# Optimization experiments

Hardware: AMD Instinct MI355X
Metric: run time of the kernel (lower is better)

The kernel has to match this reference:

```python
import jax, jax.numpy as jnp
import numpy as np

EPS = 1e-8


def setup_inputs() -> dict:
    key = jax.random.key(0)
    k1, k2, k3, k4, k5 = jax.random.split(key, 5)
    B, D, N, M = 16, 128, 2048, 2048
    return {
        "src_embedding": jax.random.normal(k1, (B, D, N), dtype=jnp.float32),
        "tgt_embedding": jax.random.normal(k2, (B, D, M), dtype=jnp.float32),
        "src": jax.random.normal(k3, (B, 3, N), dtype=jnp.float32),
        "tgt": jax.random.normal(k4, (B, 3, M), dtype=jnp.float32),
        "temperature": jax.random.uniform(k5, (B, 1), dtype=jnp.float32),
    }


def reference(src_embedding, tgt_embedding, src, tgt, temperature):
    B = src.shape[0]
    # cross-attention scores [B, N, M] and row softmax
    scores = jax.nn.softmax(
        jnp.einsum("bdn,bdm->bnm", src_embedding, tgt_embedding), axis=-1
    )
    # hard correspondence: argmax over tgt points, gather tgt coords -> [B, 3, N]
    idx = jnp.argmax(scores, axis=-1)                      # [B, N]
    src_corr = jnp.take_along_axis(tgt, idx[:, None, :].repeat(3, axis=1), axis=-1)
    # entropy-based weights (note: original applies -1/(entropy+eps), kept faithfully)
    w = jnp.sum(scores * jnp.log(scores + EPS), axis=-1)   # [B, N]
    w = -1.0 / (w + EPS)
    w_norm = w / (jnp.sum(w, axis=-1, keepdims=True) + EPS)  # [B, N]
    wn = w_norm[:, None, :]                                # [B, 1, N]
    src_centroid = jnp.sum(src * wn, axis=2, keepdims=True)       # [B, 3, 1]
    tgt_centroid = jnp.sum(src_corr * wn, axis=2, keepdims=True)  # [B, 3, 1]
    src_centered = src - src_centroid
    corr_centered = (src_corr - tgt_centroid) * wn
    # 3x3 cross-covariance per batch
    H = jnp.einsum("bin,bjn->bij", src_centered, corr_centered) + jnp.eye(3, dtype=src.dtype) * EPS
    # batched 3x3 SVD entirely on device; torch.svd returns V s.t. H = U S V^T
    U, S, Vh = jnp.linalg.svd(H)
    V = jnp.swapaxes(Vh, -1, -2)
    r = jnp.einsum("bij,bkj->bik", V, U)                   # V @ U^T
    det = jnp.linalg.det(r)                                # [B]
    diag = jnp.tile(jnp.eye(3, dtype=src.dtype), (B, 1, 1)).at[:, 2, 2].set(det)
    R = jnp.einsum("bij,bjk,blk->bil", V, diag, U)         # V @ diag @ U^T
    t = (jnp.einsum("bij,bjk->bik", -R, src_centroid) + tgt_centroid).reshape(B, 3)
    return R, t, scores
```

## Files before the change

### kernel.cpp

```cpp
#include <hip/hip_runtime.h>
#include <math.h>

constexpr int B = 16, D = 128, N = 2048, M = 2048;
#define EPSF 1e-8f

__global__ __launch_bounds__(256) void gemm_logits(
    const float* __restrict__ Ae, const float* __restrict__ Be,
    float* __restrict__ out)
{
    const int b  = blockIdx.z;
    const int n0 = blockIdx.y * 128;
    const int m0 = blockIdx.x * 128;
    const float* A  = Ae + (size_t)b * D * N;
    const float* Bm = Be + (size_t)b * D * M;
    float* C = out + (size_t)b * N * M;

    __shared__ float As[8][128];
    __shared__ float Bs[8][128];

    const int t  = threadIdx.x;
    const int lr = t >> 5;
    const int lc = (t & 31) * 4;
    const int tx = t & 15;
    const int ty = t >> 4;

    float acc[8][8];
#pragma unroll
    for (int i = 0; i < 8; ++i)
#pragma unroll
        for (int j = 0; j < 8; ++j) acc[i][j] = 0.f;

    for (int d0 = 0; d0 < D; d0 += 8) {
        const float4 av = *(const float4*)(A  + (size_t)(d0 + lr) * N + n0 + lc);
        const float4 bv = *(const float4*)(Bm + (size_t)(d0 + lr) * M + m0 + lc);
        *(float4*)(&As[lr][lc]) = av;
        *(float4*)(&Bs[lr][lc]) = bv;
        __syncthreads();
#pragma unroll
        for (int kk = 0; kk < 8; ++kk) {
            float a[8], bb[8];
            *(float4*)(&a[0])  = *(const float4*)(&As[kk][ty * 4]);
            *(float4*)(&a[4])  = *(const float4*)(&As[kk][64 + ty * 4]);
            *(float4*)(&bb[0]) = *(const float4*)(&Bs[kk][tx * 4]);
            *(float4*)(&bb[4]) = *(const float4*)(&Bs[kk][64 + tx * 4]);
#pragma unroll
            for (int i = 0; i < 8; ++i)
#pragma unroll
                for (int j = 0; j < 8; ++j)
                    acc[i][j] = fmaf(a[i], bb[j], acc[i][j]);
        }
        __syncthreads();
    }

#pragma unroll
    for (int i = 0; i < 8; ++i) {
        const int row = (i < 4) ? (ty * 4 + i) : (64 + ty * 4 + (i - 4));
        float4 c0 = make_float4(acc[i][0], acc[i][1], acc[i][2], acc[i][3]);
        float4 c1 = make_float4(acc[i][4], acc[i][5], acc[i][6], acc[i][7]);
        size_t base = (size_t)(n0 + row) * M + m0;
        *(float4*)(C + base + tx * 4)      = c0;
        *(float4*)(C + base + 64 + tx * 4) = c1;
    }
}

__global__ __launch_bounds__(256) void softmax_rows(
    float* __restrict__ scores, float* __restrict__ wout, int* __restrict__ idxout)
{
    const int row = blockIdx.x;
    float* p = scores + (size_t)row * M;
    const int t = threadIdx.x;

    float4 v0 = ((const float4*)p)[t];
    float4 v1 = ((const float4*)p)[t + 256];
    float vals[8] = {v0.x, v0.y, v0.z, v0.w, v1.x, v1.y, v1.z, v1.w};
    int   idxs[8] = {t*4, t*4+1, t*4+2, t*4+3,
                     1024 + t*4, 1024 + t*4 + 1, 1024 + t*4 + 2, 1024 + t*4 + 3};

    float m = vals[0]; int mi = idxs[0];
#pragma unroll
    for (int k = 1; k < 8; ++k)
        if (vals[k] > m) { m = vals[k]; mi = idxs[k]; }

    __shared__ float sv[256];
    __shared__ int   si[256];
    sv[t] = m; si[t] = mi;
    __syncthreads();
    for (int s = 128; s > 0; s >>= 1) {
        if (t < s) {
            float ov = sv[t + s]; int oi = si[t + s];
            if (ov > sv[t] || (ov == sv[t] && oi < si[t])) { sv[t] = ov; si[t] = oi; }
        }
        __syncthreads();
    }
    const float rowmax = sv[0];
    const int   rowidx = si[0];
    __syncthreads();

    float e[8]; float lsum = 0.f;
#pragma unroll
    for (int k = 0; k < 8; ++k) { e[k] = expf(vals[k] - rowmax); lsum += e[k]; }
    sv[t] = lsum;
    __syncthreads();
    for (int s = 128; s > 0; s >>= 1) { if (t < s) sv[t] += sv[t + s]; __syncthreads(); }
    const float inv = 1.0f / sv[0];
    __syncthreads();

    float ent = 0.f;
#pragma unroll
    for (int k = 0; k < 8; ++k) {
        float pk = e[k] * inv;
        e[k] = pk;
        ent += pk * logf(pk + EPSF);
    }
    ((float4*)p)[t]       = make_float4(e[0], e[1], e[2], e[3]);
    ((float4*)p)[t + 256] = make_float4(e[4], e[5], e[6], e[7]);

    sv[t] = ent;
    __syncthreads();
    for (int s = 128; s > 0; s >>= 1) { if (t < s) sv[t] += sv[t + s]; __syncthreads(); }
    if (t == 0) {
        wout[row]   = -1.0f / (sv[0] + EPSF);
        idxout[row] = rowidx;
    }
}

__device__ inline float block_sum_256(float v, float* red, int t)
{
    red[t] = v; __syncthreads();
    for (int s = 128; s > 0; s >>= 1) { if (t < s) red[t] += red[t + s]; __syncthreads(); }
    float r = red[0]; __syncthreads();
    return r;
}

__global__ __launch_bounds__(256) void kabsch(
    const float* __restrict__ src, const float* __restrict__ tgt,
    const float* __restrict__ wraw, const int* __restrict__ idxv,
    float* __restrict__ Rout, float* __restrict__ tout)
{
    const int b = blockIdx.x;
    const int t = threadIdx.x;
    const float* S  = src  + (size_t)b * 3 * N;
    const float* T  = tgt  + (size_t)b * 3 * M;
    const float* w  = wraw + (size_t)b * N;
    const int*  idx = idxv + (size_t)b * N;

    __shared__ float red[256];

    float w8[8]; int i8[8];
    float s8[8][3], g8[8][3];
    float lsum = 0.f;
#pragma unroll
    for (int k = 0; k < 8; ++k) {
        int n = t + 256 * k;
        w8[k] = w[n];
        i8[k] = idx[n];
        lsum += w8[k];
#pragma unroll
        for (int i = 0; i < 3; ++i) {
            s8[k][i] = S[i * N + n];
            g8[k][i] = T[i * M + i8[k]];
        }
    }
    const float W = block_sum_256(lsum, red, t) + EPSF;

    float c[6] = {0, 0, 0, 0, 0, 0};
#pragma unroll
    for (int k = 0; k < 8; ++k) {
        float wn = w8[k] / W;
#pragma unroll
        for (int i = 0; i < 3; ++i) {
            c[i]     += wn * s8[k][i];
            c[3 + i] += wn * g8[k][i];
        }
    }
    float cen[6];
    for (int i = 0; i < 6; ++i) cen[i] = block_sum_256(c[i], red, t);

    float h[9] = {0};
#pragma unroll
    for (int k = 0; k < 8; ++k) {
        float wn = w8[k] / W;
        float a0 = s8[k][0] - cen[0], a1 = s8[k][1] - cen[1], a2 = s8[k][2] - cen[2];
        float b0 = (g8[k][0] - cen[3]) * wn;
        float b1 = (g8[k][1] - cen[4]) * wn;
        float b2 = (g8[k][2] - cen[5]) * wn;
        h[0] += a0 * b0; h[1] += a0 * b1; h[2] += a0 * b2;
        h[3] += a1 * b0; h[4] += a1 * b1; h[5] += a1 * b2;
        h[6] += a2 * b0; h[7] += a2 * b1; h[8] += a2 * b2;
    }
    float hr[9];
    for (int i = 0; i < 9; ++i) hr[i] = block_sum_256(h[i], red, t);

    if (t == 0) {
        double H[3][3];
        for (int i = 0; i < 3; ++i)
            for (int j = 0; j < 3; ++j)
                H[i][j] = (double)hr[i * 3 + j] + (i == j ? 1e-8 : 0.0);

        double A[3][3];
        for (int i = 0; i < 3; ++i)
            for (int j = 0; j < 3; ++j)
                A[i][j] = H[0][i] * H[0][j] + H[1][i] * H[1][j] + H[2][i] * H[2][j];

        double V[3][3] = {{1, 0, 0}, {0, 1, 0}, {0, 0, 1}};
        const int PP[3] = {0, 0, 1}, QQ[3] = {1, 2, 2};
        for (int sweep = 0; sweep < 30; ++sweep) {
            for (int r = 0; r < 3; ++r) {
                int p = PP[r], q = QQ[r];
                double apq = A[p][q];
                if (fabs(apq) < 1e-300) continue;
                double theta = (A[q][q] - A[p][p]) / (2.0 * apq);
                double tt = (theta >= 0 ? 1.0 : -1.0) /
                            (fabs(theta) + sqrt(theta * theta + 1.0));
                double cc = 1.0 / sqrt(tt * tt + 1.0);
                double ss = tt * cc;
                for (int k = 0; k < 3; ++k) {
                    double akp = A[k][p], akq = A[k][q];
                    A[k][p] = cc * akp - ss * akq;
                    A[k][q] = ss * akp + cc * akq;
                }
                for (int k = 0; k < 3; ++k) {
                    double apk = A[p][k], aqk = A[q][k];
                    A[p][k] = cc * apk - ss * aqk;
                    A[q][k] = ss * apk + cc * aqk;
                }
                for (int k = 0; k < 3; ++k) {
                    double vkp = V[k][p], vkq = V[k][q];
                    V[k][p] = cc * vkp - ss * vkq;
                    V[k][q] = ss * vkp + cc * vkq;
                }
            }
        }
        double ev[3] = {A[0][0], A[1][1], A[2][2]};
        int ord[3] = {0, 1, 2};
        for (int i = 0; i < 2; ++i)
            for (int j = i + 1; j < 3; ++j)
                if (ev[ord[j]] > ev[ord[i]]) { int tmp = ord[i]; ord[i] = ord[j]; ord[j] = tmp; }
        double Vs[3][3];
        for (int i = 0; i < 3; ++i)
            for (int j = 0; j < 3; ++j)
                Vs[i][j] = V[i][ord[j]];

        double U[3][3];
        for (int j = 0; j < 2; ++j) {
            double u0 = H[0][0] * Vs[0][j] + H[0][1] * Vs[1][j] + H[0][2] * Vs[2][j];
            double u1 = H[1][0] * Vs[0][j] + H[1][1] * Vs[1][j] + H[1][2] * Vs[2][j];
            double u2 = H[2][0] * Vs[0][j] + H[2][1] * Vs[1][j] + H[2][2] * Vs[2][j];
            if (j == 1) {
                double d0 = u0 * U[0][0] + u1 * U[1][0] + u2 * U[2][0];
                u0 -= d0 * U[0][0]; u1 -= d0 * U[1][0]; u2 -= d0 * U[2][0];
            }
            double nn = sqrt(u0 * u0 + u1 * u1 + u2 * u2);
            if (nn < 1e-150) {
                u0 = (j == 0) ? 1.0 : -U[1][0];
                u1 = (j == 0) ? 0.0 : U[0][0];
                u2 = 0.0;
                nn = sqrt(u0 * u0 + u1 * u1 + u2 * u2);
                if (nn < 1e-150) { u0 = 0; u1 = 0; u2 = 1; nn = 1; }
            }
            U[0][j] = u0 / nn; U[1][j] = u1 / nn; U[2][j] = u2 / nn;
        }
        U[0][2] = U[1][0] * U[2][1] - U[2][0] * U[1][1];
        U[1][2] = U[2][0] * U[0][1] - U[0][0] * U[2][1];
        U[2][2] = U[0][0] * U[1][1] - U[1][0] * U[0][1];

        double r[3][3];
        for (int i = 0; i < 3; ++i)
            for (int j = 0; j < 3; ++j)
                r[i][j] = Vs[i][0] * U[j][0] + Vs[i][1] * U[j][1] + Vs[i][2] * U[j][2];
        double det = r[0][0] * (r[1][1] * r[2][2] - r[1][2] * r[2][1])
                   - r[0][1] * (r[1][0] * r[2][2] - r[1][2] * r[2][0])
                   + r[0][2] * (r[1][0] * r[2][1] - r[1][1] * r[2][0]);

        double R[3][3];
        for (int i = 0; i < 3; ++i)
            for (int j = 0; j < 3; ++j)
                R[i][j] = Vs[i][0] * U[j][0] + Vs[i][1] * U[j][1] + det * Vs[i][2] * U[j][2];

        double tv[3];
        for (int i = 0; i < 3; ++i)
            tv[i] = (double)cen[3 + i]
                  - (R[i][0] * cen[0] + R[i][1] * cen[1] + R[i][2] * cen[2]);

        for (int i = 0; i < 3; ++i)
            for (int j = 0; j < 3; ++j)
                Rout[b * 9 + i * 3 + j] = (float)R[i][j];
        for (int i = 0; i < 3; ++i)
            tout[b * 3 + i] = (float)tv[i];
    }
}

extern "C" void kernel_launch(void* const* d_in, const int* in_sizes, int n_in,
                              void* d_out, int out_size, void* d_ws, size_t ws_size,
                              hipStream_t stream)
{
    const float* src_emb = (const float*)d_in[0];
    const float* tgt_emb = (const float*)d_in[1];
    const float* src     = (const float*)d_in[2];
    const float* tgt     = (const float*)d_in[3];

    float* out    = (float*)d_out;
    float* Rout   = out;
    float* tout   = out + B * 9;
    float* scores = out + B * 12;

    float* wws   = (float*)d_ws;
    int*   idxws = (int*)((float*)d_ws + B * N);

    dim3 g1(M / 128, N / 128, B);
    gemm_logits<<<g1, 256, 0, stream>>>(src_emb, tgt_emb, scores);
    softmax_rows<<<B * N, 256, 0, stream>>>(scores, wws, idxws);
    kabsch<<<B, 256, 0, stream>>>(src, tgt, wws, idxws, Rout, tout);
}
```

Baseline: 572.1 us.

## Prefetch next GEMM tile into registers and use wave-shuffle block reductions

```diff
diff --git a/kernel.cpp b/kernel.cpp
--- a/kernel.cpp
+++ b/kernel.cpp
@@ -24,18 +24,26 @@
     const int tx = t & 15;
     const int ty = t >> 4;
 
+    const float* Aptr = A  + (size_t)lr * N + n0 + lc;
+    const float* Bptr = Bm + (size_t)lr * M + m0 + lc;
+
     float acc[8][8];
 #pragma unroll
     for (int i = 0; i < 8; ++i)
 #pragma unroll
         for (int j = 0; j < 8; ++j) acc[i][j] = 0.f;
 
+    float4 av = *(const float4*)(Aptr);
+    float4 bv = *(const float4*)(Bptr);
+
     for (int d0 = 0; d0 < D; d0 += 8) {
-        const float4 av = *(const float4*)(A  + (size_t)(d0 + lr) * N + n0 + lc);
-        const float4 bv = *(const float4*)(Bm + (size_t)(d0 + lr) * M + m0 + lc);
         *(float4*)(&As[lr][lc]) = av;
         *(float4*)(&Bs[lr][lc]) = bv;
         __syncthreads();
+        if (d0 + 8 < D) {
+            av = *(const float4*)(Aptr + (size_t)(d0 + 8) * N);
+            bv = *(const float4*)(Bptr + (size_t)(d0 + 8) * M);
+        }
 #pragma unroll
         for (int kk = 0; kk < 8; ++kk) {
             float a[8], bb[8];
@@ -69,6 +77,7 @@
     const int row = blockIdx.x;
     float* p = scores + (size_t)row * M;
     const int t = threadIdx.x;
+    const int wid = t >> 6;
 
     float4 v0 = ((const float4*)p)[t];
     float4 v1 = ((const float4*)p)[t + 256];
@@ -83,27 +92,49 @@
 
     __shared__ float sv[256];
     __shared__ int   si[256];
+    __shared__ float resf[2];
+    __shared__ int   resi;
+
     sv[t] = m; si[t] = mi;
     __syncthreads();
-    for (int s = 128; s > 0; s >>= 1) {
-        if (t < s) {
-            float ov = sv[t + s]; int oi = si[t + s];
-            if (ov > sv[t] || (ov == sv[t] && oi < si[t])) { sv[t] = ov; si[t] = oi; }
-        }
-        __syncthreads();
-    }
-    const float rowmax = sv[0];
-    const int   rowidx = si[0];
-    __syncthreads();
+    if (t < 128) {
+        float ov = sv[t + 128]; int oi = si[t + 128];
+        if (ov > m || (ov == m && oi < mi)) { m = ov; mi = oi; }
+    }
+    if (wid == 1) { sv[t] = m; si[t] = mi; }
+    __syncthreads();
+    if (t < 64) {
+        float ov = sv[t + 64]; int oi = si[t + 64];
+        if (ov > m || (ov == m && oi < mi)) { m = ov; mi = oi; }
+#pragma unroll
+        for (int s = 32; s > 0; s >>= 1) {
+            float om = __shfl_down(m, s);
+            int   oi2 = __shfl_down(mi, s);
+            if (om > m || (om == m && oi2 < mi)) { m = om; mi = oi2; }
+        }
+        if (t == 0) { resf[0] = m; resi = mi; }
+    }
+    __syncthreads();
+    const float rowmax = resf[0];
+    const int   rowidx = resi;
 
     float e[8]; float lsum = 0.f;
 #pragma unroll
     for (int k = 0; k < 8; ++k) { e[k] = expf(vals[k] - rowmax); lsum += e[k]; }
     sv[t] = lsum;
     __syncthreads();
-    for (int s = 128; s > 0; s >>= 1) { if (t < s) sv[t] += sv[t + s]; __syncthreads(); }
-    const float inv = 1.0f / sv[0];
-    __syncthreads();
+    float sum = lsum;
+    if (t < 128) sum = sum + sv[t + 128];
+    if (wid == 1) sv[t] = sum;
+    __syncthreads();
+    if (t < 64) {
+        sum = sum + sv[t + 64];
+#pragma unroll
+        for (int s = 32; s > 0; s >>= 1) sum = sum + __shfl_down(sum, s);
+        if (t == 0) resf[1] = sum;
+    }
+    __syncthreads();
+    const float inv = 1.0f / resf[1];
 
     float ent = 0.f;
 #pragma unroll
@@ -117,19 +148,51 @@
 
     sv[t] = ent;
     __syncthreads();
-    for (int s = 128; s > 0; s >>= 1) { if (t < s) sv[t] += sv[t + s]; __syncthreads(); }
-    if (t == 0) {
-        wout[row]   = -1.0f / (sv[0] + EPSF);
-        idxout[row] = rowidx;
-    }
-}
-
-__device__ inline float block_sum_256(float v, float* red, int t)
-{
-    red[t] = v; __syncthreads();
-    for (int s = 128; s > 0; s >>= 1) { if (t < s) red[t] += red[t + s]; __syncthreads(); }
-    float r = red[0]; __syncthreads();
-    return r;
+    if (t < 128) ent = ent + sv[t + 128];
+    if (wid == 1) sv[t] = ent;
+    __syncthreads();
+    if (t < 64) {
+        ent = ent + sv[t + 64];
+#pragma unroll
+        for (int s = 32; s > 0; s >>= 1) ent = ent + __shfl_down(ent, s);
+        if (t == 0) {
+            wout[row]   = -1.0f / (ent + EPSF);
+            idxout[row] = rowidx;
+        }
+    }
+}
+
+template <int Q>
+__device__ inline void block_sum_hybrid(float (&v)[Q], float (*red)[256],
+                                        float* res, int t, int wid)
+{
+#pragma unroll
+    for (int q = 0; q < Q; ++q) red[q][t] = v[q];
+    __syncthreads();
+    if (t < 128) {
+#pragma unroll
+        for (int q = 0; q < Q; ++q) v[q] += red[q][t + 128];
+    }
+    if (wid == 1) {
+#pragma unroll
+        for (int q = 0; q < Q; ++q) red[q][t] = v[q];
+    }
+    __syncthreads();
+    if (t < 64) {
+#pragma unroll
+        for (int q = 0; q < Q; ++q) v[q] += red[q][t + 64];
+#pragma unroll
+        for (int s = 32; s > 0; s >>= 1)
+#pragma unroll
+            for (int q = 0; q < Q; ++q) v[q] += __shfl_down(v[q], s);
+        if (t == 0) {
+#pragma unroll
+            for (int q = 0; q < Q; ++q) res[q] = v[q];
+        }
+    }
+    __syncthreads();
+#pragma unroll
+    for (int q = 0; q < Q; ++q) v[q] = res[q];
 }
 
 __global__ __launch_bounds__(256) void kabsch(
@@ -139,29 +202,32 @@
 {
     const int b = blockIdx.x;
     const int t = threadIdx.x;
+    const int wid = t >> 6;
     const float* S  = src  + (size_t)b * 3 * N;
     const float* T  = tgt  + (size_t)b * 3 * M;
     const float* w  = wraw + (size_t)b * N;
     const int*  idx = idxv + (size_t)b * N;
 
-    __shared__ float red[256];
+    __shared__ float red[9][256];
+    __shared__ float res[9];
 
     float w8[8]; int i8[8];
     float s8[8][3], g8[8][3];
-    float lsum = 0.f;
+    float lsum[1] = {0.f};
 #pragma unroll
     for (int k = 0; k < 8; ++k) {
         int n = t + 256 * k;
         w8[k] = w[n];
         i8[k] = idx[n];
-        lsum += w8[k];
+        lsum[0] += w8[k];
 #pragma unroll
         for (int i = 0; i < 3; ++i) {
             s8[k][i] = S[i * N + n];
             g8[k][i] = T[i * M + i8[k]];
         }
     }
-    const float W = block_sum_256(lsum, red, t) + EPSF;
+    block_sum_hybrid<1>(lsum, red, res, t, wid);
+    const float W = lsum[0] + EPSF;
 
     float c[6] = {0, 0, 0, 0, 0, 0};
 #pragma unroll
@@ -173,8 +239,10 @@
             c[3 + i] += wn * g8[k][i];
         }
     }
+    block_sum_hybrid<6>(c, red, res, t, wid);
     float cen[6];
-    for (int i = 0; i < 6; ++i) cen[i] = block_sum_256(c[i], red, t);
+#pragma unroll
+    for (int i = 0; i < 6; ++i) cen[i] = c[i];
 
     float h[9] = {0};
 #pragma unroll
@@ -188,10 +256,13 @@
         h[3] += a1 * b0; h[4] += a1 * b1; h[5] += a1 * b2;
         h[6] += a2 * b0; h[7] += a2 * b1; h[8] += a2 * b2;
     }
-    float hr[9];
-    for (int i = 0; i < 9; ++i) hr[i] = block_sum_256(h[i], red, t);
+    block_sum_hybrid<9>(h, red, res, t, wid);
 
     if (t == 0) {
+        float hr[9];
+#pragma unroll
+        for (int q = 0; q < 9; ++q) hr[q] = h[q];
+
         double H[3][3];
         for (int i = 0; i < 3; ++i)
             for (int j = 0; j < 3; ++j)
```

Measured after the change: 562.5 us. About the same (-1.7%).
